# Kernel tuning notes

Measured on AMD Instinct MI355X. Metric: run time of the kernel, lower is better.

## Reference

```python
import jax, jax.numpy as jnp
import numpy as np

LN_EPS = 1e-5


def setup_inputs() -> dict:
    key = jax.random.key(0)
    k1, k2, k3, k4, k5 = jax.random.split(key, 5)
    N, D, E, T = 100000, 128, 400000, 4  # nodes, feat dim, edges per etype, n etypes
    feat = jax.random.normal(k1, (N, D), dtype=jnp.float32)
    W = jax.random.normal(k2, (T, D, D), dtype=jnp.float32)
    Wf = jax.random.normal(k3, (T, D, 2 * D), dtype=jnp.float32)
    ln_w = jnp.ones((D,), dtype=jnp.float32)
    ln_b = jnp.zeros((D,), dtype=jnp.float32)
    src = jax.random.randint(k4, (T, E), 0, N, dtype=jnp.int32)
    dst = jax.random.randint(k5, (T, E), 0, N, dtype=jnp.int32)
    return {"feat": feat, "W": W, "Wf": Wf, "ln_w": ln_w, "ln_b": ln_b, "src": src, "dst": dst}


def reference(feat, W, Wf, ln_w, ln_b, src, dst):
    N, D = feat.shape
    T = W.shape[0]
    h = jnp.zeros((N, D), dtype=feat.dtype)
    for t in range(T):  # small fixed loop over edge types (structurally distinct weights)
        msg = feat @ W[t]                    # [N, D] per-src-node projection
        fw = feat @ Wf[t]                    # [N, 2D] FiLM params (dst ntype == src ntype)
        gamma, beta = fw[:, :D], fw[:, D:]
        m = jax.nn.relu(gamma * msg + beta)  # node-wise FiLM + ReLU, pre-scatter
        # copy_u -> gather message at edge src; fn.sum -> segment-sum into dst
        h = h + jax.ops.segment_sum(m[src[t]], dst[t], num_segments=N)
    # LayerNorm (elementwise affine); dropout omitted (eval mode)
    mu = jnp.mean(h, axis=-1, keepdims=True)
    var = jnp.mean(jnp.square(h - mu), axis=-1, keepdims=True)
    out = (h - mu) * jax.lax.rsqrt(var + LN_EPS) * ln_w + ln_b
    return out
```

## Files before the change

### kernel.cpp

```cpp
#include <hip/hip_runtime.h>
#include <hip/hip_bf16.h>

#define DD 128
#define LN_EPS 1e-5f
#define BCAP 3072
#define MAXBIN 1024
#define CHUNK 4096
#define EIDX_CAP 1024

typedef __bf16 bf16x8 __attribute__((ext_vector_type(8)));
typedef float f32x4 __attribute__((ext_vector_type(4)));

__device__ __forceinline__ float bflo(unsigned int u) { return __uint_as_float(u << 16); }
__device__ __forceinline__ float bfhi(unsigned int u) { return __uint_as_float(u & 0xffff0000u); }

__device__ __forceinline__ void gload_lds16(const void* g, void* lds) {
    __builtin_amdgcn_global_load_lds(
        (const __attribute__((address_space(1))) unsigned int*)g,
        (__attribute__((address_space(3))) unsigned int*)lds, 16, 0, 0);
}

__global__ __launch_bounds__(256) void k_head(const float* __restrict__ feat,
                                              const float* __restrict__ W,
                                              const float* __restrict__ Wf,
                                              const int* __restrict__ dst,
                                              unsigned short* __restrict__ fb,
                                              unsigned short* __restrict__ wcat,
                                              int* __restrict__ H, int* __restrict__ ticket,
                                              int E4, int NBLK, int NBIN, int n8) {
    __shared__ int h[MAXBIN];
    const int b = blockIdx.x, tid = threadIdx.x;
    if (b == 0 && tid == 0) *ticket = 0;

    if (b < NBLK) {
        for (int j = tid; j < NBIN; j += 256) h[j] = 0;
        __syncthreads();
        int base = b * CHUNK;
        int end = base + CHUNK < E4 ? base + CHUNK : E4;
        for (int i = base + tid; i < end; i += 256) atomicAdd(&h[dst[i] >> 7], 1);
        __syncthreads();
        for (int j = tid; j < NBIN; j += 256) H[(size_t)j * NBLK + b] = h[j];
    }

    const int gtid = b * 256 + tid, gsz = gridDim.x * 256;

    for (int i = gtid; i < n8; i += gsz) {
        const float4* p = (const float4*)feat + (size_t)i * 2;
        float4 v0 = p[0], v1 = p[1];
        float vv[8] = {v0.x, v0.y, v0.z, v0.w, v1.x, v1.y, v1.z, v1.w};
        unsigned short u[8];
#pragma unroll
        for (int j = 0; j < 8; j++) {
            __hip_bfloat16 bb = __float2bfloat16(vv[j]);
            u[j] = *reinterpret_cast<unsigned short*>(&bb);
        }
        uint4 o;
        o.x = u[0] | ((unsigned)u[1] << 16);
        o.y = u[2] | ((unsigned)u[3] << 16);
        o.z = u[4] | ((unsigned)u[5] << 16);
        o.w = u[6] | ((unsigned)u[7] << 16);
        ((uint4*)fb)[i] = o;
    }

    for (int i = gtid; i < 4 * 384 * 128; i += gsz) {
        int t = i / (384 * 128);
        int r = i % (384 * 128);
        int c = r / 128, k = r % 128;
        float v = (c < 128) ? W[((size_t)t * 128 + k) * 128 + c]
                            : Wf[((size_t)t * 128 + k) * 256 + (c - 128)];
        __hip_bfloat16 bb = __float2bfloat16(v);
        wcat[i] = *reinterpret_cast<unsigned short*>(&bb);
    }
}

__global__ __launch_bounds__(256) void k_scanbin(int* __restrict__ H, int* __restrict__ C,
                                                 int* __restrict__ binoff,
                                                 int* __restrict__ ticket,
                                                 int NBLK, int NBIN) {
    __shared__ int s[256];
    __shared__ int is_last;
    const int wv = (blockIdx.x * 256 + threadIdx.x) >> 6;
    const int lane = threadIdx.x & 63;
    const int tid = threadIdx.x;

    if (wv < NBIN) {
        int* row = H + (size_t)wv * NBLK;
        int run = 0;
        for (int base = 0; base < NBLK; base += 64) {
            int idx = base + lane;
            int v = (idx < NBLK) ? row[idx] : 0;
            int sc = v;
#pragma unroll
            for (int o = 1; o < 64; o <<= 1) {
                int u = __shfl_up(sc, o, 64);
                if (lane >= o) sc += u;
            }
            if (idx < NBLK) row[idx] = run + sc - v;
            run += __shfl(sc, 63, 64);
        }
        if (lane == 0) C[wv] = run;
    }

    __syncthreads();
    if (tid == 0) {
        __threadfence();
        int v = atomicAdd(ticket, 1);
        is_last = (v == (int)gridDim.x - 1);
    }
    __syncthreads();
    if (!is_last) return;
    __threadfence();

    int v[4];
    int tot = 0;
#pragma unroll
    for (int j = 0; j < 4; j++) {
        int idx = tid * 4 + j;
        v[j] = (idx < NBIN) ? C[idx] : 0;
        tot += v[j];
    }
    s[tid] = tot;
    __syncthreads();
    for (int st = 1; st < 256; st <<= 1) {
        int t = s[tid];
        int add = (tid >= st) ? s[tid - st] : 0;
        __syncthreads();
        s[tid] = t + add;
        __syncthreads();
    }
    int run = s[tid] - tot;
#pragma unroll
    for (int j = 0; j < 4; j++) {
        int idx = tid * 4 + j;
        if (idx < NBIN) binoff[idx] = run;
        run += v[j];
    }
    if (tid == 255) binoff[NBIN] = s[255];
}

__global__ __launch_bounds__(256) void k_place2(const int* __restrict__ src,
                                                const int* __restrict__ dst,
                                                const int* __restrict__ H,
                                                const int* __restrict__ binoff,
                                                unsigned int* __restrict__ rec,
                                                int N, int E, int E4, int NBLK, int NBIN) {
    __shared__ int fill[MAXBIN];
    const int b = blockIdx.x;
    for (int j = threadIdx.x; j < NBIN; j += 256)
        fill[j] = binoff[j] + H[(size_t)j * NBLK + b];
    __syncthreads();
    int base = b * CHUNK;
    int end = base + CHUNK < E4 ? base + CHUNK : E4;
    for (int i = base + threadIdx.x; i < end; i += 256) {
        int d = dst[i];
        int t = i / E;
        unsigned int r = ((unsigned)(d & 127) << 19) | (unsigned)(t * N + src[i]);
        int pos = atomicAdd(&fill[d >> 7], 1);
        rec[pos] = r;
    }
}

__global__ __launch_bounds__(256) void k_sortout(const unsigned int* __restrict__ rec,
                                                 const int* __restrict__ binoff,
                                                 unsigned int* __restrict__ sortedg,
                                                 int2* __restrict__ nodemeta, int N) {
    __shared__ int lcnt[128], soff[128], sfill[128], tmp[128];
    __shared__ unsigned int sorted[BCAP];
    const int b = blockIdx.x, tid = threadIdx.x;
    const int s0 = binoff[b];
    int n = binoff[b + 1] - s0;
    if (n > BCAP) n = BCAP;

    if (tid < 128) lcnt[tid] = 0;
    __syncthreads();
    for (int j = tid; j < n; j += 256) atomicAdd(&lcnt[rec[s0 + j] >> 19], 1);
    __syncthreads();
    if (tid < 128) tmp[tid] = lcnt[tid];
    __syncthreads();
    for (int st = 1; st < 128; st <<= 1) {
        int t = 0, a = 0;
        if (tid < 128) {
            t = tmp[tid];
            a = (tid >= st) ? tmp[tid - st] : 0;
        }
        __syncthreads();
        if (tid < 128) tmp[tid] = t + a;
        __syncthreads();
    }
    if (tid < 128) {
        int ex = tmp[tid] - lcnt[tid];
        soff[tid] = ex;
        sfill[tid] = ex;
    }
    __syncthreads();
    for (int j = tid; j < n; j += 256) {
        unsigned int r = rec[s0 + j];
        int p = atomicAdd(&sfill[r >> 19], 1);
        sorted[p] = r & 0x7FFFFu;
    }
    __syncthreads();
    for (int j = tid; j < n; j += 256) sortedg[s0 + j] = sorted[j];
    if (tid < 128) {
        int node = b * 128 + tid;
        if (node < N) nodemeta[node] = make_int2(s0 + soff[tid], lcnt[tid]);
    }
}

__global__ __launch_bounds__(256, 2) void k_gemm_film(const unsigned short* __restrict__ featb,
                                                      const unsigned short* __restrict__ wcat,
                                                      unsigned short* __restrict__ m, int N,
                                                      int NT) {
    __shared__ unsigned char smem[2 * 16384];
    const int t = blockIdx.y;
    const int tid = threadIdx.x;
    const int w = tid >> 6, lane = tid & 63;
    const int lr = lane & 15, kg = lane >> 4;
    const int cbase = w * 32;

    const unsigned short* wt = wcat + (size_t)t * 384 * 128;
    bf16x8 B[4][3][2];
#pragma unroll
    for (int kkI = 0; kkI < 4; kkI++)
#pragma unroll
        for (int mat = 0; mat < 3; mat++)
#pragma unroll
            for (int cj = 0; cj < 2; cj++) {
                int col = mat * 128 + cbase + cj * 16 + lr;
                B[kkI][mat][cj] = *(const bf16x8*)(wt + (size_t)col * 128 + kkI * 32 + kg * 8);
            }

    auto stage = [&](int buf, int r0) {
#pragma unroll
        for (int it = 0; it < 4; it++) {
            int row = it * 16 + w * 4 + (lane >> 4);
            int gr = r0 + row;
            if (gr >= N) gr = N - 1;
            int x = ((lane & 15) * 16) ^ ((row & 7) << 4);
            const unsigned char* g = (const unsigned char*)featb + (size_t)gr * 256 + x;
            gload_lds16(g, smem + buf * 16384 + it * 4096 + w * 1024);
        }
    };

    unsigned short* mt = m + (size_t)t * N * DD;
    int buf = 0;
    int tile = blockIdx.x;
    if (tile < NT) stage(0, tile * 64);

    for (; tile < NT; tile += gridDim.x) {
        __syncthreads();
        int nxt = tile + gridDim.x;
        if (nxt < NT) stage(buf ^ 1, nxt * 64);

        const unsigned char* sm = smem + buf * 16384;
        f32x4 acc[4][3][2] = {};
#pragma unroll
        for (int kkI = 0; kkI < 4; kkI++) {
            bf16x8 a[4];
#pragma unroll
            for (int mi = 0; mi < 4; mi++) {
                int row = mi * 16 + lr;
                int kb = kkI * 64 + kg * 16;
                a[mi] = *(const bf16x8*)(sm + row * 256 + (kb ^ ((row & 7) << 4)));
            }
#pragma unroll
            for (int mi = 0; mi < 4; mi++)
#pragma unroll
                for (int mat = 0; mat < 3; mat++)
#pragma unroll
                    for (int cj = 0; cj < 2; cj++)
                        acc[mi][mat][cj] = __builtin_amdgcn_mfma_f32_16x16x32_bf16(
                            a[mi], B[kkI][mat][cj], acc[mi][mat][cj], 0, 0, 0);
        }

        const int r0 = tile * 64;
#pragma unroll
        for (int mi = 0; mi < 4; mi++)
#pragma unroll
            for (int cj = 0; cj < 2; cj++)
#pragma unroll
                for (int r = 0; r < 4; r++) {
                    int row = r0 + mi * 16 + kg * 4 + r;
                    if (row < N) {
                        float v = acc[mi][1][cj][r] * acc[mi][0][cj][r] + acc[mi][2][cj][r];
                        v = fmaxf(v, 0.0f);
                        __hip_bfloat16 bb = __float2bfloat16(v);
                        mt[(size_t)row * DD + cbase + cj * 16 + lr] =
                            *reinterpret_cast<unsigned short*>(&bb);
                    }
                }
        buf ^= 1;
    }
}

__global__ __launch_bounds__(256) void k_agg_ln(const unsigned int* __restrict__ sortedg,
                                                const int2* __restrict__ nodemeta,
                                                const char* __restrict__ mbase,
                                                const float* __restrict__ lnw,
                                                const float* __restrict__ lnb,
                                                float* __restrict__ out, int N) {
    __shared__ unsigned eidx[EIDX_CAP];
    __shared__ int smeta[8];
    const int wv = threadIdx.x >> 6, lane = threadIdx.x & 63;
    const int tid = threadIdx.x;
    const int node = blockIdx.x * 4 + wv;
    const int nclamp = node < N ? node : N - 1;
    const int2 meta = nodemeta[nclamp];
    if (lane == 0) {
        smeta[wv * 2] = meta.x;
        smeta[wv * 2 + 1] = meta.y;
    }
    __syncthreads();
    const int estart0 = smeta[0];
    const int total = smeta[6] + smeta[7] - estart0;
    const bool fits = (total <= EIDX_CAP);
    if (fits)
        for (int j = tid; j < total; j += 256) eidx[j] = sortedg[estart0 + j];
    __syncthreads();
    if (node >= N) return;

    const int deg = meta.y;
    const int q = lane >> 4, sl = lane & 15;
    const unsigned soff = (unsigned)sl * 16u;
    float a[8] = {0.f, 0.f, 0.f, 0.f, 0.f, 0.f, 0.f, 0.f};

    if (fits) {
        const int loff = meta.x - estart0;
        int e = 0;
        for (; e + 16 <= deg; e += 16) {
            unsigned r0 = eidx[loff + e + q];
            unsigned r1 = eidx[loff + e + 4 + q];
            unsigned r2 = eidx[loff + e + 8 + q];
            unsigned r3 = eidx[loff + e + 12 + q];
            uint4 p0 = *(const uint4*)(mbase + (r0 * 256u + soff));
            uint4 p1 = *(const uint4*)(mbase + (r1 * 256u + soff));
            uint4 p2 = *(const uint4*)(mbase + (r2 * 256u + soff));
            uint4 p3 = *(const uint4*)(mbase + (r3 * 256u + soff));
            a[0] += bflo(p0.x) + bflo(p1.x) + bflo(p2.x) + bflo(p3.x);
            a[1] += bfhi(p0.x) + bfhi(p1.x) + bfhi(p2.x) + bfhi(p3.x);
            a[2] += bflo(p0.y) + bflo(p1.y) + bflo(p2.y) + bflo(p3.y);
            a[3] += bfhi(p0.y) + bfhi(p1.y) + bfhi(p2.y) + bfhi(p3.y);
            a[4] += bflo(p0.z) + bflo(p1.z) + bflo(p2.z) + bflo(p3.z);
            a[5] += bfhi(p0.z) + bfhi(p1.z) + bfhi(p2.z) + bfhi(p3.z);
            a[6] += bflo(p0.w) + bflo(p1.w) + bflo(p2.w) + bflo(p3.w);
            a[7] += bfhi(p0.w) + bfhi(p1.w) + bfhi(p2.w) + bfhi(p3.w);
        }
        for (; e + 4 <= deg; e += 4) {
            unsigned r0 = eidx[loff + e + q];
            uint4 p0 = *(const uint4*)(mbase + (r0 * 256u + soff));
            a[0] += bflo(p0.x);
            a[1] += bfhi(p0.x);
            a[2] += bflo(p0.y);
            a[3] += bfhi(p0.y);
            a[4] += bflo(p0.z);
            a[5] += bfhi(p0.z);
            a[6] += bflo(p0.w);
            a[7] += bfhi(p0.w);
        }
        if (e < deg) {
            int idx = e + q;
            float w = (idx < deg) ? 1.0f : 0.0f;
            if (idx >= deg) idx = deg - 1;
            unsigned r0 = eidx[loff + idx];
            uint4 p0 = *(const uint4*)(mbase + (r0 * 256u + soff));
            a[0] += w * bflo(p0.x);
            a[1] += w * bfhi(p0.x);
            a[2] += w * bflo(p0.y);
            a[3] += w * bfhi(p0.y);
            a[4] += w * bflo(p0.z);
            a[5] += w * bfhi(p0.z);
            a[6] += w * bflo(p0.w);
            a[7] += w * bfhi(p0.w);
        }
    } else {
        const int start = meta.x;
        int e = 0;
        for (; e + 4 <= deg; e += 4) {
            unsigned r0 = sortedg[start + e + q];
            uint4 p0 = *(const uint4*)(mbase + (r0 * 256u + soff));
            a[0] += bflo(p0.x);
            a[1] += bfhi(p0.x);
            a[2] += bflo(p0.y);
            a[3] += bfhi(p0.y);
            a[4] += bflo(p0.z);
            a[5] += bfhi(p0.z);
            a[6] += bflo(p0.w);
            a[7] += bfhi(p0.w);
        }
        if (e < deg) {
            int idx = e + q;
            float w = (idx < deg) ? 1.0f : 0.0f;
            if (idx >= deg) idx = deg - 1;
            unsigned r0 = sortedg[start + idx];
            uint4 p0 = *(const uint4*)(mbase + (r0 * 256u + soff));
            a[0] += w * bflo(p0.x);
            a[1] += w * bfhi(p0.x);
            a[2] += w * bflo(p0.y);
            a[3] += w * bfhi(p0.y);
            a[4] += w * bflo(p0.z);
            a[5] += w * bfhi(p0.z);
            a[6] += w * bflo(p0.w);
            a[7] += w * bfhi(p0.w);
        }
    }

#pragma unroll
    for (int j = 0; j < 8; j++) {
        a[j] += __shfl_xor(a[j], 16, 64);
        a[j] += __shfl_xor(a[j], 32, 64);
    }
    float s = 0.f, ss = 0.f;
#pragma unroll
    for (int j = 0; j < 8; j++) {
        s += a[j];
        ss += a[j] * a[j];
    }
#pragma unroll
    for (int o = 1; o < 16; o <<= 1) {
        s += __shfl_xor(s, o, 64);
        ss += __shfl_xor(ss, o, 64);
    }
    float mu = s * (1.0f / 128.0f);
    float var = ss * (1.0f / 128.0f) - mu * mu;
    float rstd = rsqrtf(var + LN_EPS);
    if (q == 0) {
        float4 w0 = ((const float4*)lnw)[sl * 2];
        float4 w1 = ((const float4*)lnw)[sl * 2 + 1];
        float4 b0 = ((const float4*)lnb)[sl * 2];
        float4 b1 = ((const float4*)lnb)[sl * 2 + 1];
        float4 o0, o1;
        o0.x = (a[0] - mu) * rstd * w0.x + b0.x;
        o0.y = (a[1] - mu) * rstd * w0.y + b0.y;
        o0.z = (a[2] - mu) * rstd * w0.z + b0.z;
        o0.w = (a[3] - mu) * rstd * w0.w + b0.w;
        o1.x = (a[4] - mu) * rstd * w1.x + b1.x;
        o1.y = (a[5] - mu) * rstd * w1.y + b1.y;
        o1.z = (a[6] - mu) * rstd * w1.z + b1.z;
        o1.w = (a[7] - mu) * rstd * w1.w + b1.w;
        ((float4*)(out + (size_t)node * DD))[sl * 2] = o0;
        ((float4*)(out + (size_t)node * DD))[sl * 2 + 1] = o1;
    }
}

extern "C" void kernel_launch(void* const* d_in, const int* in_sizes, int n_in,
                              void* d_out, int out_size, void* d_ws, size_t ws_size,
                              hipStream_t stream) {
    const float* feat = (const float*)d_in[0];
    const float* W    = (const float*)d_in[1];
    const float* Wf   = (const float*)d_in[2];
    const float* lnw  = (const float*)d_in[3];
    const float* lnb  = (const float*)d_in[4];
    const int* src    = (const int*)d_in[5];
    const int* dst    = (const int*)d_in[6];
    float* out = (float*)d_out;

    const int N = in_sizes[0] / DD;
    const int E = in_sizes[5] / 4;
    const int E4 = 4 * E;
    const int NB = (N + 127) >> 7;
    const int NBLK = (E4 + CHUNK - 1) / CHUNK;
    const int NT = (N + 63) / 64;
    const int n8 = N * DD / 8;

    size_t off = 0;
    char* ws = (char*)d_ws;
    auto alloc = [&](size_t bytes) -> void* {
        void* p = ws + off;
        off += (bytes + 255) & ~(size_t)255;
        return p;
    };
    unsigned short* m     = (unsigned short*)alloc((size_t)4 * N * DD * 2);
    unsigned short* featb = (unsigned short*)alloc((size_t)N * DD * 2);
    unsigned short* wcat  = (unsigned short*)alloc((size_t)4 * 384 * 128 * 2);
    int* H      = (int*)alloc((size_t)NB * NBLK * 4);
    int* C      = (int*)alloc((size_t)NB * 4);
    int* binoff = (int*)alloc((size_t)(NB + 1) * 4);
    int* ticket = (int*)alloc(256);
    unsigned int* rec     = (unsigned int*)alloc((size_t)E4 * 4);
    unsigned int* sortedg = (unsigned int*)alloc((size_t)E4 * 4);
    int2* nodemeta = (int2*)alloc((size_t)N * 8);
    if (off > ws_size) return;

    k_head<<<2 * NBLK, 256, 0, stream>>>(feat, W, Wf, dst, featb, wcat, H, ticket,
                                         E4, NBLK, NB, n8);
    k_scanbin<<<(NB * 64 + 255) / 256, 256, 0, stream>>>(H, C, binoff, ticket, NBLK, NB);
    k_place2<<<NBLK, 256, 0, stream>>>(src, dst, H, binoff, rec, N, E, E4, NBLK, NB);
    k_sortout<<<NB, 256, 0, stream>>>(rec, binoff, sortedg, nodemeta, N);
    dim3 gg(128, 4);
    k_gemm_film<<<gg, 256, 0, stream>>>(featb, wcat, m, N, NT);
    k_agg_ln<<<(N + 3) / 4, 256, 0, stream>>>(sortedg, nodemeta,
                                              (const char*)m, lnw, lnb, out, N);
}
```

Baseline: 169.5 us.

## Fuse bin scan, placement and per-bin sort into one cooperative kernel

Merges the bin-offset scan, edge placement and per-bin counting sort into a single cooperative kernel that uses grid-wide syncs instead of three separate launches and an atomic ticket. It also swaps the MFMA operand order in the FiLM GEMM so each lane holds four consecutive columns, which lets the epilogue write packed 8-byte bf16 stores instead of scattered 2-byte stores. The goal is to remove launch gaps and inter-kernel drains and to make the message-table writes coalesced. The cooperative grid is NBLK blocks (about 391), which must all be resident at once, and each grid sync has its own cost.

```diff
diff --git a/kernel.cpp b/kernel.cpp
--- a/kernel.cpp
+++ b/kernel.cpp
@@ -1,5 +1,8 @@
 #include <hip/hip_runtime.h>
 #include <hip/hip_bf16.h>
+#include <hip/hip_cooperative_groups.h>
+
+namespace cg = cooperative_groups;
 
 #define DD 128
 #define LN_EPS 1e-5f
@@ -13,6 +16,10 @@
 
 __device__ __forceinline__ float bflo(unsigned int u) { return __uint_as_float(u << 16); }
 __device__ __forceinline__ float bfhi(unsigned int u) { return __uint_as_float(u & 0xffff0000u); }
+__device__ __forceinline__ unsigned short bfu(float v) {
+    __hip_bfloat16 b = __float2bfloat16(v);
+    return *reinterpret_cast<unsigned short*>(&b);
+}
 
 __device__ __forceinline__ void gload_lds16(const void* g, void* lds) {
     __builtin_amdgcn_global_load_lds(
@@ -26,11 +33,10 @@
                                               const int* __restrict__ dst,
                                               unsigned short* __restrict__ fb,
                                               unsigned short* __restrict__ wcat,
-                                              int* __restrict__ H, int* __restrict__ ticket,
+                                              int* __restrict__ H,
                                               int E4, int NBLK, int NBIN, int n8) {
     __shared__ int h[MAXBIN];
     const int b = blockIdx.x, tid = threadIdx.x;
-    if (b == 0 && tid == 0) *ticket = 0;
 
     if (b < NBLK) {
         for (int j = tid; j < NBIN; j += 256) h[j] = 0;
@@ -48,17 +54,11 @@
         const float4* p = (const float4*)feat + (size_t)i * 2;
         float4 v0 = p[0], v1 = p[1];
         float vv[8] = {v0.x, v0.y, v0.z, v0.w, v1.x, v1.y, v1.z, v1.w};
-        unsigned short u[8];
-#pragma unroll
-        for (int j = 0; j < 8; j++) {
-            __hip_bfloat16 bb = __float2bfloat16(vv[j]);
-            u[j] = *reinterpret_cast<unsigned short*>(&bb);
-        }
         uint4 o;
-        o.x = u[0] | ((unsigned)u[1] << 16);
-        o.y = u[2] | ((unsigned)u[3] << 16);
-        o.z = u[4] | ((unsigned)u[5] << 16);
-        o.w = u[6] | ((unsigned)u[7] << 16);
+        o.x = bfu(vv[0]) | ((unsigned)bfu(vv[1]) << 16);
+        o.y = bfu(vv[2]) | ((unsigned)bfu(vv[3]) << 16);
+        o.z = bfu(vv[4]) | ((unsigned)bfu(vv[5]) << 16);
+        o.w = bfu(vv[6]) | ((unsigned)bfu(vv[7]) << 16);
         ((uint4*)fb)[i] = o;
     }
 
@@ -68,141 +68,133 @@
         int c = r / 128, k = r % 128;
         float v = (c < 128) ? W[((size_t)t * 128 + k) * 128 + c]
                             : Wf[((size_t)t * 128 + k) * 256 + (c - 128)];
-        __hip_bfloat16 bb = __float2bfloat16(v);
-        wcat[i] = *reinterpret_cast<unsigned short*>(&bb);
-    }
-}
-
-__global__ __launch_bounds__(256) void k_scanbin(int* __restrict__ H, int* __restrict__ C,
-                                                 int* __restrict__ binoff,
-                                                 int* __restrict__ ticket,
-                                                 int NBLK, int NBIN) {
-    __shared__ int s[256];
-    __shared__ int is_last;
-    const int wv = (blockIdx.x * 256 + threadIdx.x) >> 6;
-    const int lane = threadIdx.x & 63;
-    const int tid = threadIdx.x;
-
-    if (wv < NBIN) {
-        int* row = H + (size_t)wv * NBLK;
-        int run = 0;
-        for (int base = 0; base < NBLK; base += 64) {
-            int idx = base + lane;
-            int v = (idx < NBLK) ? row[idx] : 0;
-            int sc = v;
-#pragma unroll
-            for (int o = 1; o < 64; o <<= 1) {
-                int u = __shfl_up(sc, o, 64);
-                if (lane >= o) sc += u;
+        wcat[i] = bfu(v);
+    }
+}
+
+__global__ __launch_bounds__(256) void k_prep2(const int* __restrict__ src,
+                                               const int* __restrict__ dst,
+                                               int* __restrict__ H, int* __restrict__ C,
+                                               int* __restrict__ binoff,
+                                               unsigned int* __restrict__ rec,
+                                               unsigned int* __restrict__ sortedg,
+                                               int2* __restrict__ nodemeta,
+                                               int N, int E, int E4, int NBLK, int NBIN) {
+    cg::grid_group grid = cg::this_grid();
+    __shared__ int shm[3584];
+    const int b = blockIdx.x, tid = threadIdx.x;
+
+    {
+        int bin = b * 4 + (tid >> 6);
+        int lane = tid & 63;
+        if (bin < NBIN) {
+            int* row = H + (size_t)bin * NBLK;
+            int run = 0;
+            for (int base = 0; base < NBLK; base += 64) {
+                int idx = base + lane;
+                int v = (idx < NBLK) ? row[idx] : 0;
+                int sc = v;
+#pragma unroll
+                for (int o = 1; o < 64; o <<= 1) {
+                    int u = __shfl_up(sc, o, 64);
+                    if (lane >= o) sc += u;
+                }
+                if (idx < NBLK) row[idx] = run + sc - v;
+                run += __shfl(sc, 63, 64);
             }
-            if (idx < NBLK) row[idx] = run + sc - v;
-            run += __shfl(sc, 63, 64);
-        }
-        if (lane == 0) C[wv] = run;
-    }
-
+            if (lane == 0) C[bin] = run;
+        }
+    }
+    grid.sync();
+
+    if (b == 0) {
+        int v[4];
+        int tot = 0;
+#pragma unroll
+        for (int j = 0; j < 4; j++) {
+            int idx = tid * 4 + j;
+            v[j] = (idx < NBIN) ? C[idx] : 0;
+            tot += v[j];
+        }
+        shm[tid] = tot;
+        __syncthreads();
+        for (int st = 1; st < 256; st <<= 1) {
+            int t = shm[tid];
+            int add = (tid >= st) ? shm[tid - st] : 0;
+            __syncthreads();
+            shm[tid] = t + add;
+            __syncthreads();
+        }
+        int run = shm[tid] - tot;
+#pragma unroll
+        for (int j = 0; j < 4; j++) {
+            int idx = tid * 4 + j;
+            if (idx < NBIN) binoff[idx] = run;
+            run += v[j];
+        }
+        if (tid == 255) binoff[NBIN] = shm[255];
+    }
+    grid.sync();
+
+    for (int j = tid; j < NBIN; j += 256) shm[j] = binoff[j] + H[(size_t)j * NBLK + b];
     __syncthreads();
-    if (tid == 0) {
-        __threadfence();
-        int v = atomicAdd(ticket, 1);
-        is_last = (v == (int)gridDim.x - 1);
-    }
-    __syncthreads();
-    if (!is_last) return;
-    __threadfence();
-
-    int v[4];
-    int tot = 0;
-#pragma unroll
-    for (int j = 0; j < 4; j++) {
-        int idx = tid * 4 + j;
-        v[j] = (idx < NBIN) ? C[idx] : 0;
-        tot += v[j];
-    }
-    s[tid] = tot;
-    __syncthreads();
-    for (int st = 1; st < 256; st <<= 1) {
-        int t = s[tid];
-        int add = (tid >= st) ? s[tid - st] : 0;
-        __syncthreads();
-        s[tid] = t + add;
-        __syncthreads();
-    }
-    int run = s[tid] - tot;
-#pragma unroll
-    for (int j = 0; j < 4; j++) {
-        int idx = tid * 4 + j;
-        if (idx < NBIN) binoff[idx] = run;
-        run += v[j];
-    }
-    if (tid == 255) binoff[NBIN] = s[255];
-}
-
-__global__ __launch_bounds__(256) void k_place2(const int* __restrict__ src,
-                                                const int* __restrict__ dst,
-                                                const int* __restrict__ H,
-                                                const int* __restrict__ binoff,
-                                                unsigned int* __restrict__ rec,
-                                                int N, int E, int E4, int NBLK, int NBIN) {
-    __shared__ int fill[MAXBIN];
-    const int b = blockIdx.x;
-    for (int j = threadIdx.x; j < NBIN; j += 256)
-        fill[j] = binoff[j] + H[(size_t)j * NBLK + b];
-    __syncthreads();
-    int base = b * CHUNK;
-    int end = base + CHUNK < E4 ? base + CHUNK : E4;
-    for (int i = base + threadIdx.x; i < end; i += 256) {
-        int d = dst[i];
-        int t = i / E;
-        unsigned int r = ((unsigned)(d & 127) << 19) | (unsigned)(t * N + src[i]);
-        int pos = atomicAdd(&fill[d >> 7], 1);
-        rec[pos] = r;
-    }
-}
-
-__global__ __launch_bounds__(256) void k_sortout(const unsigned int* __restrict__ rec,
-                                                 const int* __restrict__ binoff,
-                                                 unsigned int* __restrict__ sortedg,
-                                                 int2* __restrict__ nodemeta, int N) {
-    __shared__ int lcnt[128], soff[128], sfill[128], tmp[128];
-    __shared__ unsigned int sorted[BCAP];
-    const int b = blockIdx.x, tid = threadIdx.x;
-    const int s0 = binoff[b];
-    int n = binoff[b + 1] - s0;
-    if (n > BCAP) n = BCAP;
-
-    if (tid < 128) lcnt[tid] = 0;
-    __syncthreads();
-    for (int j = tid; j < n; j += 256) atomicAdd(&lcnt[rec[s0 + j] >> 19], 1);
-    __syncthreads();
-    if (tid < 128) tmp[tid] = lcnt[tid];
-    __syncthreads();
-    for (int st = 1; st < 128; st <<= 1) {
-        int t = 0, a = 0;
+    {
+        int base = b * CHUNK;
+        int end = base + CHUNK < E4 ? base + CHUNK : E4;
+        for (int i = base + tid; i < end; i += 256) {
+            int d = dst[i];
+            int t = i / E;
+            unsigned int r = ((unsigned)(d & 127) << 19) | (unsigned)(t * N + src[i]);
+            int pos = atomicAdd(&shm[d >> 7], 1);
+            rec[pos] = r;
+        }
+    }
+    grid.sync();
+
+    int* lcnt = shm;
+    int* soff = shm + 128;
+    int* sfill = shm + 256;
+    int* tmp = shm + 384;
+    unsigned int* sorted = (unsigned int*)(shm + 512);
+    for (int bin = b; bin < NBIN; bin += gridDim.x) {
+        __syncthreads();
+        const int s0 = binoff[bin];
+        int n = binoff[bin + 1] - s0;
+        if (n > BCAP) n = BCAP;
+
+        if (tid < 128) lcnt[tid] = 0;
+        __syncthreads();
+        for (int j = tid; j < n; j += 256) atomicAdd(&lcnt[rec[s0 + j] >> 19], 1);
+        __syncthreads();
+        if (tid < 128) tmp[tid] = lcnt[tid];
+        __syncthreads();
+        for (int st = 1; st < 128; st <<= 1) {
+            int t = 0, a = 0;
+            if (tid < 128) {
+                t = tmp[tid];
+                a = (tid >= st) ? tmp[tid - st] : 0;
+            }
+            __syncthreads();
+            if (tid < 128) tmp[tid] = t + a;
+            __syncthreads();
+        }
         if (tid < 128) {
-            t = tmp[tid];
-            a = (tid >= st) ? tmp[tid - st] : 0;
-        }
-        __syncthreads();
-        if (tid < 128) tmp[tid] = t + a;
-        __syncthreads();
-    }
-    if (tid < 128) {
-        int ex = tmp[tid] - lcnt[tid];
-        soff[tid] = ex;
-        sfill[tid] = ex;
-    }
-    __syncthreads();
-    for (int j = tid; j < n; j += 256) {
-        unsigned int r = rec[s0 + j];
-        int p = atomicAdd(&sfill[r >> 19], 1);
-        sorted[p] = r & 0x7FFFFu;
-    }
-    __syncthreads();
-    for (int j = tid; j < n; j += 256) sortedg[s0 + j] = sorted[j];
-    if (tid < 128) {
-        int node = b * 128 + tid;
-        if (node < N) nodemeta[node] = make_int2(s0 + soff[tid], lcnt[tid]);
+            int ex = tmp[tid] - lcnt[tid];
+            soff[tid] = ex;
+            sfill[tid] = ex;
+        }
+        __syncthreads();
+        for (int j = tid; j < n; j += 256) {
+            unsigned int r = rec[s0 + j];
+            int p = atomicAdd(&sfill[r >> 19], 1);
+            sorted[p] = r & 0x7FFFFu;
+        }
+        __syncthreads();
+        for (int j = tid; j < n; j += 256) sortedg[s0 + j] = sorted[j];
+        if (tid < 128) {
+            int node = bin * 128 + tid;
+            if (node < N) nodemeta[node] = make_int2(s0 + soff[tid], lcnt[tid]);
+        }
     }
 }
 
@@ -269,25 +261,28 @@
 #pragma unroll
                     for (int cj = 0; cj < 2; cj++)
                         acc[mi][mat][cj] = __builtin_amdgcn_mfma_f32_16x16x32_bf16(
-                            a[mi], B[kkI][mat][cj], acc[mi][mat][cj], 0, 0, 0);
+                            B[kkI][mat][cj], a[mi], acc[mi][mat][cj], 0, 0, 0);
         }
 
         const int r0 = tile * 64;
 #pragma unroll
-        for (int mi = 0; mi < 4; mi++)
-#pragma unroll
-            for (int cj = 0; cj < 2; cj++)
-#pragma unroll
-                for (int r = 0; r < 4; r++) {
-                    int row = r0 + mi * 16 + kg * 4 + r;
-                    if (row < N) {
-                        float v = acc[mi][1][cj][r] * acc[mi][0][cj][r] + acc[mi][2][cj][r];
-                        v = fmaxf(v, 0.0f);
-                        __hip_bfloat16 bb = __float2bfloat16(v);
-                        mt[(size_t)row * DD + cbase + cj * 16 + lr] =
-                            *reinterpret_cast<unsigned short*>(&bb);
-                    }
+        for (int mi = 0; mi < 4; mi++) {
+            int row = r0 + mi * 16 + lr;
+            if (row < N) {
+                unsigned char* rowp = (unsigned char*)mt + (size_t)row * 256;
+#pragma unroll
+                for (int cj = 0; cj < 2; cj++) {
+                    float v0 = fmaxf(acc[mi][1][cj][0] * acc[mi][0][cj][0] + acc[mi][2][cj][0], 0.0f);
+                    float v1 = fmaxf(acc[mi][1][cj][1] * acc[mi][0][cj][1] + acc[mi][2][cj][1], 0.0f);
+                    float v2 = fmaxf(acc[mi][1][cj][2] * acc[mi][0][cj][2] + acc[mi][2][cj][2], 0.0f);
+                    float v3 = fmaxf(acc[mi][1][cj][3] * acc[mi][0][cj][3] + acc[mi][2][cj][3], 0.0f);
+                    uint2 pkd;
+                    pkd.x = bfu(v0) | ((unsigned)bfu(v1) << 16);
+                    pkd.y = bfu(v2) | ((unsigned)bfu(v3) << 16);
+                    *(uint2*)(rowp + (cbase + cj * 16 + kg * 4) * 2) = pkd;
                 }
+            }
+        }
         buf ^= 1;
     }
 }
@@ -453,13 +448,13 @@
     const int* dst    = (const int*)d_in[6];
     float* out = (float*)d_out;
 
-    const int N = in_sizes[0] / DD;
-    const int E = in_sizes[5] / 4;
-    const int E4 = 4 * E;
-    const int NB = (N + 127) >> 7;
-    const int NBLK = (E4 + CHUNK - 1) / CHUNK;
-    const int NT = (N + 63) / 64;
-    const int n8 = N * DD / 8;
+    int N = in_sizes[0] / DD;
+    int E = in_sizes[5] / 4;
+    int E4 = 4 * E;
+    int NB = (N + 127) >> 7;
+    int NBLK = (E4 + CHUNK - 1) / CHUNK;
+    int NT = (N + 63) / 64;
+    int n8 = N * DD / 8;
 
     size_t off = 0;
     char* ws = (char*)d_ws;
@@ -474,17 +469,19 @@
     int* H      = (int*)alloc((size_t)NB * NBLK * 4);
     int* C      = (int*)alloc((size_t)NB * 4);
     int* binoff = (int*)alloc((size_t)(NB + 1) * 4);
-    int* ticket = (int*)alloc(256);
     unsigned int* rec     = (unsigned int*)alloc((size_t)E4 * 4);
     unsigned int* sortedg = (unsigned int*)alloc((size_t)E4 * 4);
     int2* nodemeta = (int2*)alloc((size_t)N * 8);
     if (off > ws_size) return;
 
-    k_head<<<2 * NBLK, 256, 0, stream>>>(feat, W, Wf, dst, featb, wcat, H, ticket,
+    k_head<<<2 * NBLK, 256, 0, stream>>>(feat, W, Wf, dst, featb, wcat, H,
                                          E4, NBLK, NB, n8);
-    k_scanbin<<<(NB * 64 + 255) / 256, 256, 0, stream>>>(H, C, binoff, ticket, NBLK, NB);
-    k_place2<<<NBLK, 256, 0, stream>>>(src, dst, H, binoff, rec, N, E, E4, NBLK, NB);
-    k_sortout<<<NB, 256, 0, stream>>>(rec, binoff, sortedg, nodemeta, N);
+    {
+        void* args[] = {(void*)&src, (void*)&dst, (void*)&H, (void*)&C, (void*)&binoff,
+                        (void*)&rec, (void*)&sortedg, (void*)&nodemeta,
+                        (void*)&N, (void*)&E, (void*)&E4, (void*)&NBLK, (void*)&NB};
+        hipLaunchCooperativeKernel((void*)k_prep2, dim3(NBLK), dim3(256), args, 0, stream);
+    }
     dim3 gg(128, 4);
     k_gemm_film<<<gg, 256, 0, stream>>>(featb, wcat, m, N, NT);
     k_agg_ln<<<(N + 3) / 4, 256, 0, stream>>>(sortedg, nodemeta,
```

Measured after the change: 308.7 us. 1.82x slower.
